# Kernel optimization log

Hardware: AMD Instinct MI355X
Metric: run time of the kernel (lower is better)

The kernel has to match this reference:

```python
import jax, jax.numpy as jnp
import numpy as np

V, H, L, NH, MAXS = 32000, 1024, 6, 16, 2048
HD = H // NH
FF = 4 * H
EPS = 1e-5


def _ln(x, s, b):
    m = jnp.mean(x, axis=-1, keepdims=True)
    v = jnp.mean(jnp.square(x - m), axis=-1, keepdims=True)
    return (x - m) * jax.lax.rsqrt(v + EPS) * s + b


def setup_inputs() -> dict:
    key = jax.random.key(0)
    ks = jax.random.split(key, 12)
    s = 0.02
    inp = {
        "input_ids": jax.random.randint(ks[0], (2, 1024), 0, V, dtype=jnp.int64),
        "token_emb": jax.random.normal(ks[1], (V, H), jnp.float32) * s,
        "pos_emb": jax.random.normal(ks[2], (MAXS, H), jnp.float32) * s,
        "ln1_s": jnp.ones((L, H), jnp.float32),
        "ln1_b": jnp.zeros((L, H), jnp.float32),
        "qkv_w": jax.random.normal(ks[3], (L, H, 3 * H), jnp.float32) * s,
        "qkv_b": jnp.zeros((L, 3 * H), jnp.float32),
        "out_w": jax.random.normal(ks[4], (L, H, H), jnp.float32) * s,
        "out_b": jnp.zeros((L, H), jnp.float32),
        "ln2_s": jnp.ones((L, H), jnp.float32),
        "ln2_b": jnp.zeros((L, H), jnp.float32),
        "w1": jax.random.normal(ks[5], (L, H, FF), jnp.float32) * s,
        "b1": jnp.zeros((L, FF), jnp.float32),
        "w2": jax.random.normal(ks[6], (L, FF, H), jnp.float32) * s,
        "b2": jnp.zeros((L, H), jnp.float32),
        "lnf_s": jnp.ones((H,), jnp.float32),
        "lnf_b": jnp.zeros((H,), jnp.float32),
        "lm_w": jax.random.normal(ks[7], (H, V), jnp.float32) * s,
    }
    return inp


def reference(input_ids, token_emb, pos_emb, ln1_s, ln1_b, qkv_w, qkv_b,
              out_w, out_b, ln2_s, ln2_b, w1, b1, w2, b2, lnf_s, lnf_b, lm_w):
    B, S = input_ids.shape
    x = token_emb[input_ids] + pos_emb[:S][None]  # [B,S,H]; dropout = identity (eval)
    for i in range(L):
        # --- attention block ---
        h = _ln(x, ln1_s[i], ln1_b[i])
        qkv = h @ qkv_w[i] + qkv_b[i]                      # [B,S,3H]
        q, k, v = jnp.split(qkv, 3, axis=-1)
        q = q.reshape(B, S, NH, HD)
        k = k.reshape(B, S, NH, HD)
        v = v.reshape(B, S, NH, HD)
        scores = jnp.einsum('bqhd,bkhd->bhqk', q, k) / jnp.sqrt(jnp.float32(HD))
        attn = jax.nn.softmax(scores, axis=-1)             # non-causal, as in source
        o = jnp.einsum('bhqk,bkhd->bqhd', attn, v).reshape(B, S, H)
        x = x + o @ out_w[i] + out_b[i]
        # --- mlp block ---
        h = _ln(x, ln2_s[i], ln2_b[i])
        h = jax.nn.gelu(h @ w1[i] + b1[i], approximate=False)
        x = x + h @ w2[i] + b2[i]
    x = _ln(x, lnf_s, lnf_b)
    logits = x @ lm_w                                      # [B,S,V]
    return logits
```

## Files before the change

kernel.cpp:

```cpp
#include <hip/hip_runtime.h>
#include <hip/hip_bf16.h>
#include <cstdint>
#include <cstddef>

typedef __bf16 bf16;
typedef __attribute__((ext_vector_type(8))) __bf16 bf16x8;
typedef __attribute__((ext_vector_type(4))) __bf16 bf16x4;
typedef __attribute__((ext_vector_type(4))) float f32x4;

__device__ __forceinline__ f32x4 mfma16(bf16x8 a, bf16x8 b, f32x4 c) {
    return __builtin_amdgcn_mfma_f32_16x16x32_bf16(a, b, c, 0, 0, 0);
}

__device__ __forceinline__ void async_copy16(const void* g, void* l) {
    __builtin_amdgcn_global_load_lds((const __attribute__((address_space(1))) void*)g,
                                     (__attribute__((address_space(3))) void*)l,
                                     16, 0, 0);
}

template<int Ncnt> __device__ __forceinline__ void waitv();
template<> __device__ __forceinline__ void waitv<0>() { asm volatile("s_waitcnt vmcnt(0)" ::: "memory"); }
template<> __device__ __forceinline__ void waitv<2>() { asm volatile("s_waitcnt vmcnt(2)" ::: "memory"); }
template<> __device__ __forceinline__ void waitv<3>() { asm volatile("s_waitcnt vmcnt(3)" ::: "memory"); }
template<> __device__ __forceinline__ void waitv<4>() { asm volatile("s_waitcnt vmcnt(4)" ::: "memory"); }

__device__ __forceinline__ void wait_g(int n) {
    if (n == 2) waitv<2>();
    else if (n == 3) waitv<3>();
    else waitv<4>();
}

__global__ __launch_bounds__(256)
void embed_kernel(const int* __restrict__ ids, const float* __restrict__ te,
                  const float* __restrict__ pe, float* __restrict__ x)
{
    const int row = blockIdx.x;
    const int s = row & 1023;
    const int id = ids[row];
    const f32x4* a = (const f32x4*)(te + (size_t)id * 1024);
    const f32x4* b = (const f32x4*)(pe + (size_t)s * 1024);
    f32x4* o = (f32x4*)(x + (size_t)row * 1024);
    o[threadIdx.x] = a[threadIdx.x] + b[threadIdx.x];
}

__device__ __forceinline__ void ln_body(const float* __restrict__ x, const float* __restrict__ sc,
                                        const float* __restrict__ bi, bf16* __restrict__ out,
                                        int row, int t, float* red)
{
    const f32x4 v = ((const f32x4*)(x + (size_t)row * 1024))[t];
    float s = v[0] + v[1] + v[2] + v[3];
    float q = v[0]*v[0] + v[1]*v[1] + v[2]*v[2] + v[3]*v[3];
    #pragma unroll
    for (int o = 1; o < 64; o <<= 1) { s += __shfl_xor(s, o); q += __shfl_xor(q, o); }
    const int wv = t >> 6, lane = t & 63;
    if (lane == 0) { red[wv] = s; red[4 + wv] = q; }
    __syncthreads();
    s = red[0] + red[1] + red[2] + red[3];
    q = red[4] + red[5] + red[6] + red[7];
    const float mean = s * (1.f / 1024.f);
    const float var  = q * (1.f / 1024.f) - mean * mean;
    const float rstd = rsqrtf(var + 1e-5f);
    const f32x4 scv = ((const f32x4*)sc)[t];
    const f32x4 biv = ((const f32x4*)bi)[t];
    bf16x4 o4;
    #pragma unroll
    for (int j = 0; j < 4; j++) o4[j] = (bf16)((v[j] - mean) * rstd * scv[j] + biv[j]);
    *(bf16x4*)(out + (size_t)row * 1024 + t * 4) = o4;
}

__device__ __forceinline__ void wcvt_body(const float* __restrict__ W, bf16* __restrict__ BT,
                                          int K, int N, int bid, int tidx, float (*tile)[65])
{
    const int nx = N >> 6;
    const int n0 = (bid % nx) << 6, k0 = (bid / nx) << 6;
    const int tx = tidx & 15, ty = tidx >> 4;
    #pragma unroll
    for (int r = 0; r < 4; r++) {
        const f32x4 v = *(const f32x4*)&W[(size_t)(k0 + ty + r*16) * N + n0 + tx*4];
        tile[ty + r*16][tx*4 + 0] = v[0];
        tile[ty + r*16][tx*4 + 1] = v[1];
        tile[ty + r*16][tx*4 + 2] = v[2];
        tile[ty + r*16][tx*4 + 3] = v[3];
    }
    __syncthreads();
    #pragma unroll
    for (int r = 0; r < 4; r++) {
        const int n = ty + r*16;
        bf16x4 o;
        #pragma unroll
        for (int j = 0; j < 4; j++) o[j] = (bf16)tile[tx*4 + j][n];
        *(bf16x4*)&BT[(size_t)(n0 + n) * K + k0 + tx*4] = o;
    }
}

__global__ __launch_bounds__(256)
void front_kernel(const float* __restrict__ x, const float* __restrict__ sc,
                  const float* __restrict__ bi, bf16* __restrict__ out,
                  const float* __restrict__ qkvw0, bf16* __restrict__ wTq,
                  const float* __restrict__ lmw, bf16* __restrict__ wTlm,
                  const float* __restrict__ outw, bf16* __restrict__ wTo_all)
{
    __shared__ float tile[64][65];
    __shared__ float red[8];
    const int bid = blockIdx.x, t = threadIdx.x;
    if (bid < 2048) {
        ln_body(x, sc, bi, out, bid, t, red);
    } else if (bid < 2048 + 768) {
        wcvt_body(qkvw0, wTq, 1024, 3072, bid - 2048, t, tile);
    } else if (bid < 2048 + 768 + 8000) {
        wcvt_body(lmw, wTlm, 1024, 32000, bid - 2816, t, tile);
    } else {
        const int wb = bid - 10816;
        const int l = wb >> 8;
        wcvt_body(outw + (size_t)l * 1024 * 1024, wTo_all + (size_t)l * 1024 * 1024,
                  1024, 1024, wb & 255, t, tile);
    }
}

__global__ __launch_bounds__(256)
void fused_ln_wcvt(const float* __restrict__ x, const float* __restrict__ sc,
                   const float* __restrict__ bi, bf16* __restrict__ out,
                   const float* __restrict__ W1, bf16* __restrict__ BT1, int K1, int N1, int nb1,
                   const float* __restrict__ W2, bf16* __restrict__ BT2, int K2, int N2)
{
    __shared__ float tile[64][65];
    __shared__ float red[8];
    const int bid = blockIdx.x, t = threadIdx.x;
    if (bid < 2048) {
        ln_body(x, sc, bi, out, bid, t, red);
    } else {
        const int wb = bid - 2048;
        if (wb < nb1) wcvt_body(W1, BT1, K1, N1, wb, t, tile);
        else          wcvt_body(W2, BT2, K2, N2, wb - nb1, t, tile);
    }
}

__global__ __launch_bounds__(256)
void attn_kernel(const bf16* __restrict__ qkv, const bf16* __restrict__ vT,
                 bf16* __restrict__ attno)
{
    __shared__ __align__(16) bf16 Ksh[128 * 64];
    __shared__ __align__(16) bf16 Vt[64 * 128];
    __shared__ __align__(16) bf16 Plds[4][16][132];

    const int bid = blockIdx.x, tid = threadIdx.x;
    const int b = (bid & 31) >> 4, h = bid & 15;
    const int qb = bid >> 5;
    const int lane = tid & 63, wave = tid >> 6;
    const bf16* base = qkv + (size_t)b * 1024 * 3072;
    const bf16* vbase = vT + (size_t)(b*16 + h) * 64 * 1024;
    const int qrow0 = qb * 64 + wave * 16;
    const int l15 = lane & 15;

    bf16x8 aQ[2];
    {
        const int qr = qrow0 + l15;
        const bf16* qp = base + (size_t)qr * 3072 + h * 64 + ((lane >> 4) << 3);
        aQ[0] = *(const bf16x8*)qp;
        aQ[1] = *(const bf16x8*)(qp + 32);
    }
    float m_i[4] = {-1e30f, -1e30f, -1e30f, -1e30f};
    float l_i[4] = {0.f, 0.f, 0.f, 0.f};
    f32x4 acc[4];
    #pragma unroll
    for (int nb = 0; nb < 4; nb++) acc[nb] = f32x4{0.f, 0.f, 0.f, 0.f};

    const int swzA = (((lane >> 4)     ^ (lane & 7)) << 3);
    const int swzB = (((4 + (lane >> 4)) ^ (lane & 7)) << 3);

    for (int ck = 0; ck < 8; ck++) {
        __syncthreads();
        #pragma unroll
        for (int p = 0; p < 4; p++) {
            const int c = p * 256 + tid;
            const int rw = c >> 3;
            const int kc = (c & 7) ^ (rw & 7);
            async_copy16(base + (size_t)(ck*128 + rw) * 3072 + 1024 + h*64 + kc*8, &Ksh[c * 8]);
        }
        #pragma unroll
        for (int p = 0; p < 4; p++) {
            const int c = p * 256 + tid;
            const int rw = c >> 4;
            const int kc = (c & 15) ^ (rw & 7);
            async_copy16(vbase + (size_t)rw * 1024 + ck*128 + kc*8, &Vt[c * 8]);
        }
        __syncthreads();

        f32x4 sc[8];
        #pragma unroll
        for (int kk = 0; kk < 4; kk++) {
            const int kr0 = (kk*32 + l15) * 64;
            const int kr1 = kr0 + 16*64;
            f32x4 z{0.f, 0.f, 0.f, 0.f};
            z = mfma16(aQ[0], *(const bf16x8*)&Ksh[kr0 + swzA], z);
            z = mfma16(aQ[1], *(const bf16x8*)&Ksh[kr0 + swzB], z);
            sc[2*kk] = z;
            f32x4 z2{0.f, 0.f, 0.f, 0.f};
            z2 = mfma16(aQ[0], *(const bf16x8*)&Ksh[kr1 + swzA], z2);
            z2 = mfma16(aQ[1], *(const bf16x8*)&Ksh[kr1 + swzB], z2);
            sc[2*kk+1] = z2;
        }

        float c[4];
        #pragma unroll
        for (int i = 0; i < 4; i++) {
            float t = sc[0][i];
            #pragma unroll
            for (int e = 1; e < 8; e++) t = fmaxf(t, sc[e][i]);
            #pragma unroll
            for (int o = 1; o < 16; o <<= 1) t = fmaxf(t, __shfl_xor(t, o));
            t *= 0.125f;
            const float mnew = fmaxf(m_i[i], t);
            c[i] = __expf(m_i[i] - mnew);
            float p[8];
            float rs = 0.f;
            #pragma unroll
            for (int e = 0; e < 8; e++) {
                p[e] = __expf(fmaf(sc[e][i], 0.125f, -mnew));
                rs += p[e];
            }
            #pragma unroll
            for (int o = 1; o < 16; o <<= 1) rs += __shfl_xor(rs, o);
            l_i[i] = l_i[i] * c[i] + rs;
            m_i[i] = mnew;
            const int pr = ((lane >> 4) << 2) + i;
            #pragma unroll
            for (int e = 0; e < 8; e++)
                Plds[wave][pr][(e >> 1) * 32 + (e & 1) * 16 + l15] = (bf16)p[e];
        }
        #pragma unroll
        for (int nb = 0; nb < 4; nb++) {
            f32x4 a = acc[nb];
            a[0] *= c[0]; a[1] *= c[1]; a[2] *= c[2]; a[3] *= c[3];
            acc[nb] = a;
        }

        #pragma unroll
        for (int kk = 0; kk < 4; kk++) {
            const bf16x8 aP = *(const bf16x8*)&Plds[wave][l15][kk*32 + ((lane >> 4) << 3)];
            #pragma unroll
            for (int nb = 0; nb < 4; nb++) {
                const int r = nb*16 + l15;
                const int chk = (kk*4 + (lane >> 4)) ^ (r & 7);
                const bf16x8 bV = *(const bf16x8*)&Vt[r*128 + chk*8];
                acc[nb] = mfma16(aP, bV, acc[nb]);
            }
        }
    }
    #pragma unroll
    for (int nb = 0; nb < 4; nb++) {
        #pragma unroll
        for (int i = 0; i < 4; i++) {
            const int row = qrow0 + ((lane >> 4) << 2) + i;
            const float o = acc[nb][i] / l_i[i];
            attno[(size_t)(b*1024 + row) * 1024 + h*64 + nb*16 + l15] = (bf16)o;
        }
    }
}

template<int BM, int BN, int EPI, int KSPLIT>
__global__ __launch_bounds__(512, 2)
void gemm256_kernel(const bf16* __restrict__ A, const bf16* __restrict__ BT,
                    const float* __restrict__ bias, float* __restrict__ resid,
                    bf16* __restrict__ outb, float* __restrict__ outf,
                    bf16* __restrict__ vt, int N, int K)
{
    constexpr int MT = 2048 / BM;
    constexpr int FM = BM / 32;
    constexpr int FN = BN / 64;
    constexpr int HM = FM / 2;
    constexpr int ACH = BM * 4;
    constexpr int BCH = BN * 4;
    constexpr int LA = (ACH + 511) >> 9;
    constexpr int LB = (BCH + 511) >> 9;
    constexpr int ASUB = BM * 32;
    constexpr int BSUB = BN * 32;
    extern __shared__ __align__(16) char smem_raw[];
    bf16* smem = (bf16*)smem_raw;

    const int nwg = gridDim.x;
    const int q = nwg >> 3, rr = nwg & 7;
    const int xcd = blockIdx.x & 7, ix = blockIdx.x >> 3;
    const int nid = (xcd < rr ? xcd * (q + 1) : rr * (q + 1) + (xcd - rr) * q) + ix;
    const int tiles = nwg / KSPLIT;
    const int ks = nid / tiles;
    const int tile = nid % tiles;
    const int bm = tile % MT, bn = tile / MT;

    const int tid = threadIdx.x, lane = tid & 63, wave = tid >> 6;
    const int wr = wave >> 2, wc = wave & 3;

    const int myB = ((BCH & 511) == 0) ? (BCH >> 9)
                    : ((tid < (BCH & 511)) ? (BCH >> 9) + 1 : (BCH >> 9));
    const int wcount = LA + myB;

    f32x4 acc[FM][FN];
    #pragma unroll
    for (int m = 0; m < FM; m++)
        #pragma unroll
        for (int n = 0; n < FN; n++) acc[m][n] = f32x4{0.f, 0.f, 0.f, 0.f};

    const bf16* Abase = A  + (size_t)bm * BM * K;
    const bf16* Bbase = BT + (size_t)bn * BN * K;
    const int Ts = (K >> 6) / KSPLIT;
    const int t0 = ks * Ts;

    const int l15 = lane & 15;
    const int swz = (((lane >> 4) ^ ((l15 >> 1) & 3)) << 3);
    const int arow0 = wr * (BM / 2) + l15;
    const int brow0 = wc * (BN / 4) + l15;

#define ABASE_(p_, ks_) (((p_)*2 + (ks_)) * ASUB)
#define BBASE_(p_, ks_) (4*ASUB + ((p_)*2 + (ks_)) * BSUB)
#define STAGE_A(p_, kt_, ks_) { _Pragma("unroll") for (int i = 0; i < LA; i++) { \
    const int c = tid + i * 512; \
    if ((ACH & 511) == 0 || c < ACH) { \
      const int rw = c >> 2; \
      const int kc = (c & 3) ^ ((rw >> 1) & 3); \
      async_copy16(Abase + (size_t)rw * K + (kt_)*64 + (ks_)*32 + kc*8, \
                   &smem[ABASE_(p_, ks_) + c*8]); } } }
#define STAGE_B(p_, kt_, ks_) { _Pragma("unroll") for (int i = 0; i < LB; i++) { \
    const int c = tid + i * 512; \
    if ((BCH & 511) == 0 || c < BCH) { \
      const int rw = c >> 2; \
      const int kc = (c & 3) ^ ((rw >> 1) & 3); \
      async_copy16(Bbase + (size_t)rw * K + (kt_)*64 + (ks_)*32 + kc*8, \
                   &smem[BBASE_(p_, ks_) + c*8]); } } }
#define LOAD_B(p_, ks_) { _Pragma("unroll") for (int n = 0; n < FN; n++) \
    bfv[n] = *(const bf16x8*)&smem[BBASE_(p_, ks_) + (brow0 + n*16)*32 + swz]; }
#define LOAD_A(p_, ks_, mg) { _Pragma("unroll") for (int m = 0; m < HM; m++) \
    af[m] = *(const bf16x8*)&smem[ABASE_(p_, ks_) + (arow0 + ((mg)*HM + m)*16)*32 + swz]; }
#define QUAD(mg) { __builtin_amdgcn_s_setprio(1); \
    _Pragma("unroll") for (int m = 0; m < HM; m++) \
      _Pragma("unroll") for (int n = 0; n < FN; n++) \
        acc[(mg)*HM + m][n] = mfma16(af[m], bfv[n], acc[(mg)*HM + m][n]); \
    __builtin_amdgcn_s_setprio(0); }

    STAGE_A(0, t0, 0); STAGE_B(0, t0, 0); STAGE_A(0, t0, 1); STAGE_B(0, t0, 1);
    wait_g(wcount);
    __builtin_amdgcn_s_barrier();

    for (int tl = 0; tl < Ts; tl++) {
        const int b = tl & 1;
        const int kt1 = t0 + tl + 1;
        const bool more = (tl + 1) < Ts;
        bf16x8 af[HM], bfv[FN];
        LOAD_B(b, 0); LOAD_A(b, 0, 0);
        if (more) STAGE_A(b ^ 1, kt1, 0);
        __builtin_amdgcn_s_barrier();
        QUAD(0);
        __builtin_amdgcn_s_barrier();
        LOAD_A(b, 0, 1);
        if (more) STAGE_B(b ^ 1, kt1, 0);
        __builtin_amdgcn_s_barrier();
        QUAD(1);
        if (more) wait_g(wcount); else waitv<0>();
        __builtin_amdgcn_s_barrier();
        LOAD_B(b, 1); LOAD_A(b, 1, 0);
        if (more) STAGE_A(b ^ 1, kt1, 1);
        __builtin_amdgcn_s_barrier();
        QUAD(0);
        __builtin_amdgcn_s_barrier();
        LOAD_A(b, 1, 1);
        if (more) STAGE_B(b ^ 1, kt1, 1);
        __builtin_amdgcn_s_barrier();
        QUAD(1);
        if (more) wait_g(wcount);
        __builtin_amdgcn_s_barrier();
    }

    const int er = bm * BM + wr * (BM / 2) + ((lane >> 4) << 2);
    const int ec = bn * BN + wc * (BN / 4) + l15;
    #pragma unroll
    for (int n = 0; n < FN; n++) {
        const int col = ec + n * 16;
        const float bv = (EPI == 3) ? 0.f : ((KSPLIT > 1 && ks != 0) ? 0.f : bias[col]);
        #pragma unroll
        for (int m = 0; m < FM; m++) {
            const int row0 = er + m * 16;
            if constexpr (EPI == 4) {
                if (col < 2048) {
                    #pragma unroll
                    for (int i = 0; i < 4; i++)
                        outb[(size_t)(row0 + i) * N + col] = (bf16)(acc[m][n][i] + bv);
                } else {
                    bf16x4 o4;
                    #pragma unroll
                    for (int i = 0; i < 4; i++) o4[i] = (bf16)(acc[m][n][i] + bv);
                    const int b_ = row0 >> 10, tok = row0 & 1023;
                    *(bf16x4*)&vt[((size_t)(b_ * 1024 + (col - 2048))) * 1024 + tok] = o4;
                }
            } else {
                #pragma unroll
                for (int i = 0; i < 4; i++) {
                    const float v = acc[m][n][i] + bv;
                    const size_t off = (size_t)(row0 + i) * N + col;
                    if constexpr (EPI == 0) outb[off] = (bf16)v;
                    else if constexpr (EPI == 1) {
                        if constexpr (KSPLIT > 1) atomicAdd(&resid[off], v);
                        else resid[off] += v;
                    }
                    else if constexpr (EPI == 2) {
                        outb[off] = (bf16)(0.5f * v * (1.f + erff(v * 0.70710678118f)));
                    } else {
                        outf[off] = v;
                    }
                }
            }
        }
    }
#undef ABASE_
#undef BBASE_
#undef STAGE_A
#undef STAGE_B
#undef LOAD_A
#undef LOAD_B
#undef QUAD
}

extern "C" void kernel_launch(void* const* d_in, const int* in_sizes, int n_in,
                              void* d_out, int out_size, void* d_ws, size_t ws_size,
                              hipStream_t stream)
{
    const int*   ids     = (const int*)  d_in[0];
    const float* tok_emb = (const float*)d_in[1];
    const float* pos_emb = (const float*)d_in[2];
    const float* ln1_s   = (const float*)d_in[3];
    const float* ln1_b   = (const float*)d_in[4];
    const float* qkv_w   = (const float*)d_in[5];
    const float* qkv_b   = (const float*)d_in[6];
    const float* out_w   = (const float*)d_in[7];
    const float* out_b   = (const float*)d_in[8];
    const float* ln2_s   = (const float*)d_in[9];
    const float* ln2_b   = (const float*)d_in[10];
    const float* w1      = (const float*)d_in[11];
    const float* b1      = (const float*)d_in[12];
    const float* w2      = (const float*)d_in[13];
    const float* b2      = (const float*)d_in[14];
    const float* lnf_s   = (const float*)d_in[15];
    const float* lnf_b   = (const float*)d_in[16];
    const float* lm_w    = (const float*)d_in[17];

    char* ws = (char*)d_ws;
    float* x    = (float*)ws;  ws += (size_t)2048 * 1024 * 4;
    bf16*  h    = (bf16*)ws;   ws += (size_t)2048 * 1024 * 2;
    bf16*  qkvb = (bf16*)ws;   ws += (size_t)2048 * 3072 * 2;
    bf16*  attno= (bf16*)ws;   ws += (size_t)2048 * 1024 * 2;
    bf16*  vT   = (bf16*)ws;   ws += (size_t)32 * 64 * 1024 * 2;
    bf16*  ff   = (bf16*)ws;   ws += (size_t)2048 * 4096 * 2;
    bf16*  wTq  = (bf16*)ws;   ws += (size_t)3072 * 1024 * 2;
    bf16*  wTo_all = (bf16*)ws; ws += (size_t)6 * 1024 * 1024 * 2;
    bf16*  wT1  = (bf16*)ws;   ws += (size_t)4096 * 1024 * 2;
    bf16*  wT2  = (bf16*)ws;   ws += (size_t)1024 * 4096 * 2;
    bf16*  wTlm = (bf16*)ws;   ws += (size_t)32000 * 1024 * 2;

    embed_kernel<<<2048, 256, 0, stream>>>(ids, tok_emb, pos_emb, x);

    for (int l = 0; l < 6; l++) {
        if (l == 0) {
            front_kernel<<<12352, 256, 0, stream>>>(
                x, ln1_s, ln1_b, h,
                qkv_w, wTq, lm_w, wTlm, out_w, wTo_all);
        } else {
            fused_ln_wcvt<<<2048 + 768, 256, 0, stream>>>(
                x, ln1_s + l*1024, ln1_b + l*1024, h,
                qkv_w + (size_t)l*1024*3072, wTq, 1024, 3072, 768,
                nullptr, nullptr, 0, 0);
        }
        gemm256_kernel<128,192,4,1><<<256, 512, 81920, stream>>>(
            h, wTq, qkv_b + l*3072, nullptr, qkvb, nullptr, vT, 3072, 1024);
        attn_kernel<<<512, 256, 0, stream>>>(qkvb, vT, attno);
        gemm256_kernel<128,256,1,4><<<256, 512, 98304, stream>>>(
            attno, wTo_all + (size_t)l*1024*1024, out_b + l*1024, x, nullptr, nullptr, nullptr, 1024, 1024);
        fused_ln_wcvt<<<2048 + 1024 + 1024, 256, 0, stream>>>(
            x, ln2_s + l*1024, ln2_b + l*1024, h,
            w1 + (size_t)l*1024*4096, wT1, 1024, 4096, 1024,
            w2 + (size_t)l*4096*1024, wT2, 4096, 1024);
        gemm256_kernel<128,256,2,1><<<256, 512, 98304, stream>>>(
            h, wT1, b1 + l*4096, nullptr, ff, nullptr, nullptr, 4096, 1024);
        gemm256_kernel<128,256,1,4><<<256, 512, 98304, stream>>>(
            ff, wT2, b2 + l*1024, x, nullptr, nullptr, nullptr, 1024, 4096);
    }
    fused_ln_wcvt<<<2048, 256, 0, stream>>>(
        x, lnf_s, lnf_b, h,
        nullptr, nullptr, 0, 0, 0,
        nullptr, nullptr, 0, 0);
    gemm256_kernel<256,256,3,1><<<8*125, 512, 131072, stream>>>(
        h, wTlm, nullptr, nullptr, nullptr, (float*)d_out, nullptr, 32000, 1024);
}
```

Baseline: 1.304 ms.

## Double query rows per attention wave, split K/V waits, fuse embedding into front kernel

```diff
diff --git a/kernel.cpp b/kernel.cpp
--- a/kernel.cpp
+++ b/kernel.cpp
@@ -30,24 +30,10 @@
     else waitv<4>();
 }
 
-__global__ __launch_bounds__(256)
-void embed_kernel(const int* __restrict__ ids, const float* __restrict__ te,
-                  const float* __restrict__ pe, float* __restrict__ x)
-{
-    const int row = blockIdx.x;
-    const int s = row & 1023;
-    const int id = ids[row];
-    const f32x4* a = (const f32x4*)(te + (size_t)id * 1024);
-    const f32x4* b = (const f32x4*)(pe + (size_t)s * 1024);
-    f32x4* o = (f32x4*)(x + (size_t)row * 1024);
-    o[threadIdx.x] = a[threadIdx.x] + b[threadIdx.x];
-}
-
-__device__ __forceinline__ void ln_body(const float* __restrict__ x, const float* __restrict__ sc,
-                                        const float* __restrict__ bi, bf16* __restrict__ out,
-                                        int row, int t, float* red)
-{
-    const f32x4 v = ((const f32x4*)(x + (size_t)row * 1024))[t];
+__device__ __forceinline__ void ln_vec(f32x4 v, const float* __restrict__ sc,
+                                       const float* __restrict__ bi, bf16* __restrict__ out,
+                                       int row, int t, float* red)
+{
     float s = v[0] + v[1] + v[2] + v[3];
     float q = v[0]*v[0] + v[1]*v[1] + v[2]*v[2] + v[3]*v[3];
     #pragma unroll
@@ -68,6 +54,14 @@
     *(bf16x4*)(out + (size_t)row * 1024 + t * 4) = o4;
 }
 
+__device__ __forceinline__ void ln_body(const float* __restrict__ x, const float* __restrict__ sc,
+                                        const float* __restrict__ bi, bf16* __restrict__ out,
+                                        int row, int t, float* red)
+{
+    const f32x4 v = ((const f32x4*)(x + (size_t)row * 1024))[t];
+    ln_vec(v, sc, bi, out, row, t, red);
+}
+
 __device__ __forceinline__ void wcvt_body(const float* __restrict__ W, bf16* __restrict__ BT,
                                           int K, int N, int bid, int tidx, float (*tile)[65])
 {
@@ -94,8 +88,10 @@
 }
 
 __global__ __launch_bounds__(256)
-void front_kernel(const float* __restrict__ x, const float* __restrict__ sc,
-                  const float* __restrict__ bi, bf16* __restrict__ out,
+void front_kernel(const int* __restrict__ ids, const float* __restrict__ te,
+                  const float* __restrict__ pe, float* __restrict__ x,
+                  const float* __restrict__ sc, const float* __restrict__ bi,
+                  bf16* __restrict__ out,
                   const float* __restrict__ qkvw0, bf16* __restrict__ wTq,
                   const float* __restrict__ lmw, bf16* __restrict__ wTlm,
                   const float* __restrict__ outw, bf16* __restrict__ wTo_all)
@@ -104,7 +100,13 @@
     __shared__ float red[8];
     const int bid = blockIdx.x, t = threadIdx.x;
     if (bid < 2048) {
-        ln_body(x, sc, bi, out, bid, t, red);
+        const int s = bid & 1023;
+        const int id = ids[bid];
+        const f32x4 a = ((const f32x4*)(te + (size_t)id * 1024))[t];
+        const f32x4 b = ((const f32x4*)(pe + (size_t)s * 1024))[t];
+        const f32x4 v = a + b;
+        ((f32x4*)(x + (size_t)bid * 1024))[t] = v;
+        ln_vec(v, sc, bi, out, bid, t, red);
     } else if (bid < 2048 + 768) {
         wcvt_body(qkvw0, wTq, 1024, 3072, bid - 2048, t, tile);
     } else if (bid < 2048 + 768 + 8000) {
@@ -141,7 +143,7 @@
 {
     __shared__ __align__(16) bf16 Ksh[128 * 64];
     __shared__ __align__(16) bf16 Vt[64 * 128];
-    __shared__ __align__(16) bf16 Plds[4][16][132];
+    __shared__ __align__(16) bf16 Plds[4][32][132];
 
     const int bid = blockIdx.x, tid = threadIdx.x;
     const int b = (bid & 31) >> 4, h = bid & 15;
@@ -149,21 +151,27 @@
     const int lane = tid & 63, wave = tid >> 6;
     const bf16* base = qkv + (size_t)b * 1024 * 3072;
     const bf16* vbase = vT + (size_t)(b*16 + h) * 64 * 1024;
-    const int qrow0 = qb * 64 + wave * 16;
+    const int qrow0 = qb * 128 + wave * 32;
     const int l15 = lane & 15;
-
-    bf16x8 aQ[2];
-    {
-        const int qr = qrow0 + l15;
-        const bf16* qp = base + (size_t)qr * 3072 + h * 64 + ((lane >> 4) << 3);
-        aQ[0] = *(const bf16x8*)qp;
-        aQ[1] = *(const bf16x8*)(qp + 32);
-    }
-    float m_i[4] = {-1e30f, -1e30f, -1e30f, -1e30f};
-    float l_i[4] = {0.f, 0.f, 0.f, 0.f};
-    f32x4 acc[4];
-    #pragma unroll
-    for (int nb = 0; nb < 4; nb++) acc[nb] = f32x4{0.f, 0.f, 0.f, 0.f};
+    const int hi8 = (lane >> 4) << 3;
+
+    bf16x8 aQ[2][2];
+    #pragma unroll
+    for (int rg = 0; rg < 2; rg++) {
+        const int qr = qrow0 + rg * 16 + l15;
+        const bf16* qp = base + (size_t)qr * 3072 + h * 64 + hi8;
+        aQ[rg][0] = *(const bf16x8*)qp;
+        aQ[rg][1] = *(const bf16x8*)(qp + 32);
+    }
+    float m_i[2][4], l_i[2][4];
+    f32x4 acc[2][4];
+    #pragma unroll
+    for (int rg = 0; rg < 2; rg++)
+        #pragma unroll
+        for (int i = 0; i < 4; i++) {
+            m_i[rg][i] = -1e30f; l_i[rg][i] = 0.f;
+            acc[rg][i] = f32x4{0.f, 0.f, 0.f, 0.f};
+        }
 
     const int swzA = (((lane >> 4)     ^ (lane & 7)) << 3);
     const int swzB = (((4 + (lane >> 4)) ^ (lane & 7)) << 3);
@@ -184,78 +192,101 @@
             const int kc = (c & 15) ^ (rw & 7);
             async_copy16(vbase + (size_t)rw * 1024 + ck*128 + kc*8, &Vt[c * 8]);
         }
-        __syncthreads();
-
-        f32x4 sc[8];
+        waitv<4>();
+        __builtin_amdgcn_sched_barrier(0);
+        __builtin_amdgcn_s_barrier();
+
+        f32x4 sc[2][8];
         #pragma unroll
         for (int kk = 0; kk < 4; kk++) {
             const int kr0 = (kk*32 + l15) * 64;
             const int kr1 = kr0 + 16*64;
-            f32x4 z{0.f, 0.f, 0.f, 0.f};
-            z = mfma16(aQ[0], *(const bf16x8*)&Ksh[kr0 + swzA], z);
-            z = mfma16(aQ[1], *(const bf16x8*)&Ksh[kr0 + swzB], z);
-            sc[2*kk] = z;
-            f32x4 z2{0.f, 0.f, 0.f, 0.f};
-            z2 = mfma16(aQ[0], *(const bf16x8*)&Ksh[kr1 + swzA], z2);
-            z2 = mfma16(aQ[1], *(const bf16x8*)&Ksh[kr1 + swzB], z2);
-            sc[2*kk+1] = z2;
-        }
-
-        float c[4];
-        #pragma unroll
-        for (int i = 0; i < 4; i++) {
-            float t = sc[0][i];
+            const bf16x8 kA0 = *(const bf16x8*)&Ksh[kr0 + swzA];
+            const bf16x8 kB0 = *(const bf16x8*)&Ksh[kr0 + swzB];
+            const bf16x8 kA1 = *(const bf16x8*)&Ksh[kr1 + swzA];
+            const bf16x8 kB1 = *(const bf16x8*)&Ksh[kr1 + swzB];
             #pragma unroll
-            for (int e = 1; e < 8; e++) t = fmaxf(t, sc[e][i]);
+            for (int rg = 0; rg < 2; rg++) {
+                f32x4 z{0.f, 0.f, 0.f, 0.f};
+                z = mfma16(aQ[rg][0], kA0, z);
+                z = mfma16(aQ[rg][1], kB0, z);
+                sc[rg][2*kk] = z;
+                f32x4 z2{0.f, 0.f, 0.f, 0.f};
+                z2 = mfma16(aQ[rg][0], kA1, z2);
+                z2 = mfma16(aQ[rg][1], kB1, z2);
+                sc[rg][2*kk+1] = z2;
+            }
+        }
+
+        float c[2][4];
+        #pragma unroll
+        for (int rg = 0; rg < 2; rg++) {
             #pragma unroll
-            for (int o = 1; o < 16; o <<= 1) t = fmaxf(t, __shfl_xor(t, o));
-            t *= 0.125f;
-            const float mnew = fmaxf(m_i[i], t);
-            c[i] = __expf(m_i[i] - mnew);
-            float p[8];
-            float rs = 0.f;
+            for (int i = 0; i < 4; i++) {
+                float t = sc[rg][0][i];
+                #pragma unroll
+                for (int e = 1; e < 8; e++) t = fmaxf(t, sc[rg][e][i]);
+                #pragma unroll
+                for (int o = 1; o < 16; o <<= 1) t = fmaxf(t, __shfl_xor(t, o));
+                t *= 0.125f;
+                const float mnew = fmaxf(m_i[rg][i], t);
+                c[rg][i] = __expf(m_i[rg][i] - mnew);
+                float p[8];
+                float rs = 0.f;
+                #pragma unroll
+                for (int e = 0; e < 8; e++) {
+                    p[e] = __expf(fmaf(sc[rg][e][i], 0.125f, -mnew));
+                    rs += p[e];
+                }
+                #pragma unroll
+                for (int o = 1; o < 16; o <<= 1) rs += __shfl_xor(rs, o);
+                l_i[rg][i] = l_i[rg][i] * c[rg][i] + rs;
+                m_i[rg][i] = mnew;
+                const int pr = rg * 16 + ((lane >> 4) << 2) + i;
+                #pragma unroll
+                for (int e = 0; e < 8; e++)
+                    Plds[wave][pr][(e >> 1) * 32 + (e & 1) * 16 + l15] = (bf16)p[e];
+            }
+        }
+
+        waitv<0>();
+        __builtin_amdgcn_sched_barrier(0);
+        __builtin_amdgcn_s_barrier();
+
+        #pragma unroll
+        for (int rg = 0; rg < 2; rg++)
             #pragma unroll
-            for (int e = 0; e < 8; e++) {
-                p[e] = __expf(fmaf(sc[e][i], 0.125f, -mnew));
-                rs += p[e];
+            for (int nb = 0; nb < 4; nb++) {
+                f32x4 a = acc[rg][nb];
+                a[0] *= c[rg][0]; a[1] *= c[rg][1]; a[2] *= c[rg][2]; a[3] *= c[rg][3];
+                acc[rg][nb] = a;
             }
-            #pragma unroll
-            for (int o = 1; o < 16; o <<= 1) rs += __shfl_xor(rs, o);
-            l_i[i] = l_i[i] * c[i] + rs;
-            m_i[i] = mnew;
-            const int pr = ((lane >> 4) << 2) + i;
-            #pragma unroll
-            for (int e = 0; e < 8; e++)
-                Plds[wave][pr][(e >> 1) * 32 + (e & 1) * 16 + l15] = (bf16)p[e];
-        }
-        #pragma unroll
-        for (int nb = 0; nb < 4; nb++) {
-            f32x4 a = acc[nb];
-            a[0] *= c[0]; a[1] *= c[1]; a[2] *= c[2]; a[3] *= c[3];
-            acc[nb] = a;
-        }
 
         #pragma unroll
         for (int kk = 0; kk < 4; kk++) {
-            const bf16x8 aP = *(const bf16x8*)&Plds[wave][l15][kk*32 + ((lane >> 4) << 3)];
+            const bf16x8 aP0 = *(const bf16x8*)&Plds[wave][l15][kk*32 + hi8];
+            const bf16x8 aP1 = *(const bf16x8*)&Plds[wave][16 + l15][kk*32 + hi8];
             #pragma unroll
             for (int nb = 0; nb < 4; nb++) {
                 const int r = nb*16 + l15;
                 const int chk = (kk*4 + (lane >> 4)) ^ (r & 7);
                 const bf16x8 bV = *(const bf16x8*)&Vt[r*128 + chk*8];
-                acc[nb] = mfma16(aP, bV, acc[nb]);
+                acc[0][nb] = mfma16(aP0, bV, acc[0][nb]);
+                acc[1][nb] = mfma16(aP1, bV, acc[1][nb]);
             }
         }
     }
     #pragma unroll
-    for (int nb = 0; nb < 4; nb++) {
-        #pragma unroll
-        for (int i = 0; i < 4; i++) {
-            const int row = qrow0 + ((lane >> 4) << 2) + i;
-            const float o = acc[nb][i] / l_i[i];
-            attno[(size_t)(b*1024 + row) * 1024 + h*64 + nb*16 + l15] = (bf16)o;
-        }
-    }
+    for (int rg = 0; rg < 2; rg++)
+        #pragma unroll
+        for (int nb = 0; nb < 4; nb++) {
+            #pragma unroll
+            for (int i = 0; i < 4; i++) {
+                const int row = qrow0 + rg * 16 + ((lane >> 4) << 2) + i;
+                const float o = acc[rg][nb][i] / l_i[rg][i];
+                attno[(size_t)(b*1024 + row) * 1024 + h*64 + nb*16 + l15] = (bf16)o;
+            }
+        }
 }
 
 template<int BM, int BN, int EPI, int KSPLIT>
@@ -454,12 +485,10 @@
     bf16*  wT2  = (bf16*)ws;   ws += (size_t)1024 * 4096 * 2;
     bf16*  wTlm = (bf16*)ws;   ws += (size_t)32000 * 1024 * 2;
 
-    embed_kernel<<<2048, 256, 0, stream>>>(ids, tok_emb, pos_emb, x);
-
     for (int l = 0; l < 6; l++) {
         if (l == 0) {
             front_kernel<<<12352, 256, 0, stream>>>(
-                x, ln1_s, ln1_b, h,
+                ids, tok_emb, pos_emb, x, ln1_s, ln1_b, h,
                 qkv_w, wTq, lm_w, wTlm, out_w, wTo_all);
         } else {
             fused_ln_wcvt<<<2048 + 768, 256, 0, stream>>>(
@@ -469,7 +498,7 @@
         }
         gemm256_kernel<128,192,4,1><<<256, 512, 81920, stream>>>(
             h, wTq, qkv_b + l*3072, nullptr, qkvb, nullptr, vT, 3072, 1024);
-        attn_kernel<<<512, 256, 0, stream>>>(qkvb, vT, attno);
+        attn_kernel<<<256, 256, 0, stream>>>(qkvb, vT, attno);
         gemm256_kernel<128,256,1,4><<<256, 512, 98304, stream>>>(
             attno, wTo_all + (size_t)l*1024*1024, out_b + l*1024, x, nullptr, nullptr, nullptr, 1024, 1024);
         fused_ln_wcvt<<<2048 + 1024 + 1024, 256, 0, stream>>>(
```

Result: no change. 1.324 ms (+1.6%).
